# Kernel optimization log

Hardware: AMD Instinct MI355X
Metric: run time of the kernel (lower is better)

Reference implementation:

```python
import jax, jax.numpy as jnp
import numpy as np

EPS = 1.1920929e-07  # torch clamp_probs eps for float32
TEMP = 0.3           # sampler temperature T


def conv1d(x, w, b, pad):
    # x: [B, Cin, L], w: [Cout, Cin, K] -> [B, Cout, L']
    y = jax.lax.conv_general_dilated(x, w, window_strides=(1,), padding=[(pad, pad)],
                                     dimension_numbers=('NCH', 'OIH', 'NCH'))
    return y + b[None, :, None]


def setup_inputs() -> dict:
    key = jax.random.key(0)
    ks = jax.random.split(key, 20)
    B, L, V, E, F, H, K = 512, 512, 100000, 100, 100, 100, 10
    p = lambda i, shape: jax.random.normal(ks[i], shape, jnp.float32) * 0.02
    return {
        'x': jax.random.randint(ks[0], (B, L), 0, V, dtype=jnp.int32),
        'u': jax.random.uniform(ks[1], (B, K, L), dtype=jnp.float32),
        'emb': p(2, (V, E)),
        'conv1_w': p(3, (F, E, 3)), 'conv1_b': p(4, (F,)),
        'gi_w': p(5, (H, F)), 'gi_b': p(6, (H,)),
        'conv2_w': p(7, (H, F, 3)), 'conv2_b': p(8, (H,)),
        'li_w': p(9, (H, H, 3)), 'li_b': p(10, (H,)),
        'conv3_w': p(11, (F, 2 * H, 1)), 'conv3_b': p(12, (F,)),
        'conv4_w': p(13, (1, F, 1)), 'conv4_b': p(14, (1,)),
        'fc1_w': p(15, (H, E)), 'fc1_b': p(16, (H,)),
        'head_w': p(17, (1, H)), 'head_b': p(18, (1,)),
    }


def _ti_logits(e, conv1_w, conv1_b, gi_w, gi_b, conv2_w, conv2_b,
               li_w, li_b, conv3_w, conv3_b, conv4_w, conv4_b):
    relu = jax.nn.relu
    xt = jnp.swapaxes(e, 1, 2)                       # [B, E, L]
    h = relu(conv1d(xt, conv1_w, conv1_b, 1))        # [B, F, L]
    g = relu(h.mean(axis=-1) @ gi_w.T + gi_b)        # [B, H] (AdaptiveAvgPool1d(1))
    loc = relu(conv1d(relu(conv1d(h, conv2_w, conv2_b, 1)), li_w, li_b, 1))  # [B, H, L]
    gexp = jnp.broadcast_to(g[:, :, None], loc.shape)
    z = jnp.concatenate([gexp, loc], axis=1)         # [B, 2H, L]
    z = relu(conv1d(z, conv3_w, conv3_b, 0))
    return conv1d(z, conv4_w, conv4_b, 0)            # [B, 1, L]


def reference(x, u, emb, conv1_w, conv1_b, gi_w, gi_b, conv2_w, conv2_b,
              li_w, li_b, conv3_w, conv3_b, conv4_w, conv4_b,
              fc1_w, fc1_b, head_w, head_b):
    e = emb[x]                                       # [B, L, E] embedding gather
    logits = _ti_logits(e, conv1_w, conv1_b, gi_w, gi_b, conv2_w, conv2_b,
                        li_w, li_b, conv3_w, conv3_b, conv4_w, conv4_b)
    # Gumbel top-k continuous sampling (training path)
    uc = jnp.clip(u, EPS, 1.0 - EPS)
    gumbel = -jnp.log(-jnp.log(uc))                  # [B, K, L]
    noisy = (gumbel + logits) / TEMP                 # logits [B,1,L] broadcasts over K
    csamples = jax.nn.softmax(noisy, axis=-1).max(axis=1)  # [B, L]
    # distil predictor: masked mean pooling + MLP + sigmoid head
    pooled = (e * csamples[:, :, None]).mean(axis=1)  # [B, E]
    h = jax.nn.relu(pooled @ fc1_w.T + fc1_b)
    out = jax.nn.sigmoid(h @ head_w.T + head_b)       # [B, 1]
    return out, csamples
```

## Files before the change

kernel.cpp:

```cpp
#include <hip/hip_runtime.h>
#include <math.h>

#define DEV __device__ __forceinline__

typedef __attribute__((ext_vector_type(8))) short short8;
typedef __attribute__((ext_vector_type(4))) short short4v;
typedef __attribute__((ext_vector_type(4))) float f32x4;

#define SSTR 136

DEV short f2bf(float f) {
    unsigned u = __builtin_bit_cast(unsigned, f);
    unsigned r = (u + 0x7fffu + ((u >> 16) & 1u)) >> 16;
    return (short)r;
}

__global__ __launch_bounds__(256) void emb_cvt_kernel(
    const float* __restrict__ emb, short* __restrict__ embT) {
    int t = threadIdx.x;
    int row = blockIdx.x * 8 + (t >> 5);
    int c4 = t & 31;
    if (c4 >= 28) return;
    short4v v = {0, 0, 0, 0};
    if (c4 < 25) {
        f32x4 e = *(const f32x4*)&emb[row * 100 + c4 * 4];
#pragma unroll
        for (int r = 0; r < 4; ++r) v[r] = f2bf(e[r]);
    }
    *(short4v*)&embT[row * 112 + c4 * 4] = v;
}

__global__ __launch_bounds__(64) void pack_all_kernel(
    const float* __restrict__ c1w, const float* __restrict__ c2w,
    const float* __restrict__ liw, const float* __restrict__ c3w,
    short* __restrict__ A1, short* __restrict__ A2,
    short* __restrict__ A3, short* __restrict__ A4) {
    int bx = blockIdx.x;
    const float* w; short* dst; int mode, lbx;
    if (bx < 70)       { w = c1w; dst = A1; mode = 0; lbx = bx; }
    else if (bx < 140) { w = c2w; dst = A2; mode = 0; lbx = bx - 70; }
    else if (bx < 210) { w = liw; dst = A3; mode = 0; lbx = bx - 140; }
    else               { w = c3w; dst = A4; mode = 1; lbx = bx - 210; }
    int lane = threadIdx.x;
    int f = lbx % 7 * 16 + (lane & 15);
    int kb = (lbx / 7) * 32 + (lane >> 4) * 8;
    short8 v;
#pragma unroll
    for (int j = 0; j < 8; ++j) {
        int kk = kb + j;
        float val = 0.f;
        if (f < 100) {
            if (mode == 0) {
                int oct = kk >> 3, dk = oct / 13;
                int c = (oct - 13 * dk) * 8 + (kk & 7);
                if (dk < 3 && c < 100) val = w[(f * 100 + c) * 3 + dk];
            } else {
                if (kk < 100) val = w[f * 200 + 100 + kk];
            }
        }
        v[j] = f2bf(val);
    }
    *(short8*)&dst[(lbx * 64 + lane) * 8] = v;
}

template<int NT, bool POOL, bool TO_GLOBAL>
DEV void conv3tap(const short* __restrict__ Ap, const float* __restrict__ bias,
                  const short* s_src, short* s_dst, short* __restrict__ gout,
                  int row0l, int l0, float* __restrict__ hpart, int pbase,
                  int lane, int wv) {
    const int q = lane >> 4, n = lane & 15;
    const int mt0 = wv * 2;
    const bool two = (wv < 3);
    const f32x4 z4 = {0.f, 0.f, 0.f, 0.f};
    f32x4 acc0[NT], acc1[NT];
#pragma unroll
    for (int nt = 0; nt < NT; ++nt) { acc0[nt] = z4; acc1[nt] = z4; }
#pragma unroll
    for (int ks = 0; ks < 10; ++ks) {
        short8 a0 = *(const short8*)&Ap[(ks * 448 + mt0 * 64 + lane) * 8];
        short8 a1;
        if (two) a1 = *(const short8*)&Ap[(ks * 448 + (mt0 + 1) * 64 + lane) * 8];
        int oct = ks * 4 + q;
        int dk = oct / 13;
        int c0 = (oct - 13 * dk) * 8;
        const short* bptr = s_src + (n + dk) * SSTR + c0;
#pragma unroll
        for (int nt = 0; nt < NT; ++nt) {
            short8 bf;
            if (nt < 4) {
                bf = *(const short8*)(bptr + nt * 16 * SSTR);
            } else {
                int r = 64 + n + dk; if (r > 69) r = 69;
                bf = *(const short8*)&s_src[r * SSTR + c0];
            }
            acc0[nt] = __builtin_amdgcn_mfma_f32_16x16x32_bf16(a0, bf, acc0[nt], 0, 0, 0);
            if (two)
                acc1[nt] = __builtin_amdgcn_mfma_f32_16x16x32_bf16(a1, bf, acc1[nt], 0, 0, 0);
        }
    }
    const int fb0 = mt0 * 16 + q * 4;
    const int fb1 = fb0 + 16;
    f32x4 bs0 = (fb0 < 100) ? *(const f32x4*)&bias[fb0] : z4;
    f32x4 bs1 = (two && fb1 < 100) ? *(const f32x4*)&bias[fb1] : z4;
    f32x4 ps0 = z4, ps1 = z4;
#pragma unroll
    for (int nt = 0; nt < NT; ++nt) {
        const int j = nt * 16 + n;
        const int l = row0l + j;
        const bool lok = (l >= 0) && (l < 512);
        const bool pok = (l >= l0) && (l < l0 + 64);
        short4v pk0, pk1;
#pragma unroll
        for (int r = 0; r < 4; ++r) {
            float v0 = fmaxf(acc0[nt][r] + bs0[r], 0.f);
            v0 = lok ? v0 : 0.f;
            pk0[r] = f2bf(v0);
            if constexpr (POOL) { if (pok) ps0[r] += v0; }
            if (two) {
                float v1 = fmaxf(acc1[nt][r] + bs1[r], 0.f);
                v1 = lok ? v1 : 0.f;
                pk1[r] = f2bf(v1);
                if constexpr (POOL) { if (pok) ps1[r] += v1; }
            }
        }
        if constexpr (TO_GLOBAL) {
            if (j < 64) {
                *(short4v*)&gout[j * 112 + fb0] = pk0;
                if (two) *(short4v*)&gout[j * 112 + fb1] = pk1;
            }
        } else {
            if (j < 70) {
                *(short4v*)&s_dst[j * SSTR + fb0] = pk0;
                if (two) *(short4v*)&s_dst[j * SSTR + fb1] = pk1;
            }
        }
    }
    if constexpr (POOL) {
#pragma unroll
        for (int off = 1; off <= 8; off <<= 1)
#pragma unroll
            for (int r = 0; r < 4; ++r) {
                ps0[r] += __shfl_xor(ps0[r], off, 64);
                ps1[r] += __shfl_xor(ps1[r], off, 64);
            }
        if (n == 0) {
            *(f32x4*)&hpart[pbase * 112 + fb0] = ps0;
            if (two) *(f32x4*)&hpart[pbase * 112 + fb1] = ps1;
        }
    }
}

__global__ __launch_bounds__(256, 4) void fused_conv_kernel(
    const int* __restrict__ xidx, const short* __restrict__ embT,
    const short* __restrict__ A1, const short* __restrict__ A2,
    const short* __restrict__ A3,
    const float* __restrict__ b1, const float* __restrict__ b2,
    const float* __restrict__ b3,
    short* __restrict__ locT, float* __restrict__ hpart) {
    extern __shared__ char smem[];
    short* s_e = (short*)smem;
    short* s_h = (short*)(smem + 72 * SSTR * 2);
    const int tid = threadIdx.x;
    const int b = blockIdx.y, bx = blockIdx.x, l0 = bx * 64;
    const int lane = tid & 63, wv = tid >> 6;

#pragma unroll
    for (int p = 0; p < 5; ++p) {
        int idx = tid + p * 256;
        int j = idx >> 4, c8 = idx & 15;
        if (j < 70 && c8 < 14) {
            int lg = l0 - 3 + j;
            short8 v = {0, 0, 0, 0, 0, 0, 0, 0};
            if (lg >= 0 && lg < 512) {
                int row = xidx[b * 512 + lg];
                v = *(const short8*)&embT[row * 112 + c8 * 8];
            }
            *(short8*)&s_e[j * SSTR + c8 * 8] = v;
        }
    }
    __syncthreads();
    conv3tap<5, true, false>(A1, b1, s_e, s_h, nullptr, l0 - 2, l0,
                             hpart, b * 8 + bx, lane, wv);
    __syncthreads();
    conv3tap<5, false, false>(A2, b2, s_h, s_e, nullptr, l0 - 1, l0,
                              nullptr, 0, lane, wv);
    __syncthreads();
    conv3tap<4, false, true>(A3, b3, s_e, nullptr,
                             locT + ((size_t)b * 512 + l0) * 112, l0, l0,
                             nullptr, 0, lane, wv);
}

__global__ __launch_bounds__(256, 4) void conv3_logits_kernel(
    const short* __restrict__ locT, const short* __restrict__ A4,
    const float* __restrict__ zg, const float* __restrict__ w4,
    const float* __restrict__ b4, float* __restrict__ logits) {
    extern __shared__ char smem[];
    short* s_in = (short*)smem;
    float* s_part = (float*)(smem + 128 * SSTR * 2);
    const int tid = threadIdx.x;
    const int b = blockIdx.y, l0r = blockIdx.x * 128;
    const int lane = tid & 63, wv = tid >> 6;
    const int q = lane >> 4, n = lane & 15;

    {
        short8 tmp[8];
#pragma unroll
        for (int p = 0; p < 8; ++p) {
            int idx = tid + p * 256;
            int j = idx >> 4, c8 = idx & 15;
            if (c8 < 14)
                tmp[p] = *(const short8*)&locT[((size_t)b * 512 + l0r + j) * 112 + c8 * 8];
        }
#pragma unroll
        for (int p = 0; p < 8; ++p) {
            int idx = tid + p * 256;
            int j = idx >> 4, c8 = idx & 15;
            if (c8 < 14)
                *(short8*)&s_in[j * SSTR + c8 * 8] = tmp[p];
        }
    }
    __syncthreads();

    const f32x4 z4 = {0.f, 0.f, 0.f, 0.f};
    const int mt0 = wv * 2;
    const bool two = (wv < 3);
    f32x4 acc0[8], acc1[8];
#pragma unroll
    for (int nt = 0; nt < 8; ++nt) { acc0[nt] = z4; acc1[nt] = z4; }
#pragma unroll
    for (int ks = 0; ks < 4; ++ks) {
        short8 a0 = *(const short8*)&A4[(ks * 448 + mt0 * 64 + lane) * 8];
        short8 a1;
        if (two) a1 = *(const short8*)&A4[(ks * 448 + (mt0 + 1) * 64 + lane) * 8];
        int c0 = (ks * 4 + q) * 8;
        if (c0 > 104) c0 = 104;
        const short* bptr = s_in + n * SSTR + c0;
#pragma unroll
        for (int nt = 0; nt < 8; ++nt) {
            short8 bf = *(const short8*)(bptr + nt * 16 * SSTR);
            acc0[nt] = __builtin_amdgcn_mfma_f32_16x16x32_bf16(a0, bf, acc0[nt], 0, 0, 0);
            if (two)
                acc1[nt] = __builtin_amdgcn_mfma_f32_16x16x32_bf16(a1, bf, acc1[nt], 0, 0, 0);
        }
    }
    const int fb0 = mt0 * 16 + q * 4, fb1 = fb0 + 16;
    f32x4 w40 = (fb0 < 100) ? *(const f32x4*)&w4[fb0] : z4;
    f32x4 w41 = (two && fb1 < 100) ? *(const f32x4*)&w4[fb1] : z4;
    f32x4 zg0 = *(const f32x4*)&zg[b * 112 + fb0];
    f32x4 zg1 = two ? *(const f32x4*)&zg[b * 112 + fb1] : z4;
#pragma unroll
    for (int nt = 0; nt < 8; ++nt) {
        float part = 0.f;
#pragma unroll
        for (int r = 0; r < 4; ++r) {
            part += fmaxf(acc0[nt][r] + zg0[r], 0.f) * w40[r];
            if (two) part += fmaxf(acc1[nt][r] + zg1[r], 0.f) * w41[r];
        }
        part += __shfl_xor(part, 16, 64);
        part += __shfl_xor(part, 32, 64);
        if (q == 0) s_part[wv * 128 + nt * 16 + n] = part;
    }
    __syncthreads();
    if (tid < 128) {
        float s = s_part[tid] + s_part[128 + tid] + s_part[256 + tid] +
                  s_part[384 + tid] + b4[0];
        logits[b * 512 + l0r + tid] = s;
    }
}

__global__ __launch_bounds__(128) void pool_gate_kernel(
    const float* __restrict__ hpart, const float* __restrict__ gi_w,
    const float* __restrict__ gi_b, const float* __restrict__ w3,
    const float* __restrict__ b3, float* __restrict__ zg) {
    int b = blockIdx.x, tid = threadIdx.x;
    __shared__ float s_hm[112];
    __shared__ float s_g[100];
    if (tid < 112) {
        float a = 0.f;
#pragma unroll
        for (int s = 0; s < 8; ++s) a += hpart[(b * 8 + s) * 112 + tid];
        s_hm[tid] = a * (1.f / 512.f);
    }
    __syncthreads();
    if (tid < 100) {
        float a = gi_b[tid];
        for (int f = 0; f < 100; ++f) a += s_hm[f] * gi_w[tid * 100 + f];
        s_g[tid] = fmaxf(a, 0.f);
    }
    __syncthreads();
    if (tid < 112) {
        float a = 0.f;
        if (tid < 100) {
            a = b3[tid];
            for (int h = 0; h < 100; ++h) a += s_g[h] * w3[tid * 200 + h];
        }
        zg[b * 112 + tid] = a;
    }
}

__global__ __launch_bounds__(256) void sampler_kernel(
    const float* __restrict__ u, const float* __restrict__ logits,
    float* __restrict__ cs) {
    const float EPSV = 1.1920929e-07f;
    int b = blockIdx.x, tid = threadIdx.x;
    int lane = tid & 63, wv = tid >> 6;
    __shared__ float s_log[512], s_cs[512], s_red[8];
    float uu[20];
#pragma unroll
    for (int k = 0; k < 10; ++k) {
        uu[k * 2]     = u[(b * 10 + k) * 512 + tid];
        uu[k * 2 + 1] = u[(b * 10 + k) * 512 + tid + 256];
    }
    for (int l = tid; l < 512; l += 256) { s_log[l] = logits[b * 512 + l]; s_cs[l] = 0.f; }
    __syncthreads();
    for (int k = 0; k < 10; ++k) {
        float nz[2];
#pragma unroll
        for (int i = 0; i < 2; ++i) {
            int l = tid + i * 256;
            float vv = fminf(fmaxf(uu[k * 2 + i], EPSV), 1.f - EPSV);
            float g = -__logf(-__logf(vv));
            nz[i] = (g + s_log[l]) * (1.f / 0.3f);
        }
        float m = fmaxf(nz[0], nz[1]);
#pragma unroll
        for (int off = 32; off >= 1; off >>= 1) m = fmaxf(m, __shfl_xor(m, off, 64));
        if (lane == 0) s_red[wv] = m;
        __syncthreads();
        m = fmaxf(fmaxf(s_red[0], s_red[1]), fmaxf(s_red[2], s_red[3]));
        float e0 = __expf(nz[0] - m), e1 = __expf(nz[1] - m);
        float s = e0 + e1;
#pragma unroll
        for (int off = 32; off >= 1; off >>= 1) s += __shfl_xor(s, off, 64);
        if (lane == 0) s_red[4 + wv] = s;
        __syncthreads();
        float inv = 1.f / (s_red[4] + s_red[5] + s_red[6] + s_red[7]);
        s_cs[tid]       = fmaxf(s_cs[tid],       e0 * inv);
        s_cs[tid + 256] = fmaxf(s_cs[tid + 256], e1 * inv);
    }
    for (int l = tid; l < 512; l += 256) cs[b * 512 + l] = s_cs[l];
}

__global__ __launch_bounds__(256) void head_part_kernel(
    const int* __restrict__ xidx, const float* __restrict__ emb,
    const float* __restrict__ cs, float* __restrict__ hp) {
    int sb = blockIdx.x, b = blockIdx.y;
    int tid = threadIdx.x;
    __shared__ int s_x[64];
    __shared__ float s_c[64];
    __shared__ float s_acc[8][104];
    if (tid < 64) {
        int l = sb * 64 + tid;
        s_x[tid] = xidx[b * 512 + l];
        s_c[tid] = cs[b * 512 + l];
    }
    __syncthreads();
    int s = tid & 31, lq = tid >> 5;
    if (s < 25) {
        f32x4 a = {0.f, 0.f, 0.f, 0.f};
#pragma unroll
        for (int i = 0; i < 8; ++i) {
            int ll = lq * 8 + i;
            int row = s_x[ll];
            float cv = s_c[ll];
            f32x4 ev = *(const f32x4*)&emb[row * 100 + s * 4];
#pragma unroll
            for (int r = 0; r < 4; ++r) a[r] += ev[r] * cv;
        }
        *(f32x4*)&s_acc[lq][s * 4] = a;
    }
    __syncthreads();
    if (tid < 100) {
        float v = 0.f;
#pragma unroll
        for (int j = 0; j < 8; ++j) v += s_acc[j][tid];
        hp[(b * 8 + sb) * 100 + tid] = v;
    }
}

__global__ __launch_bounds__(128) void head_fin_kernel(
    const float* __restrict__ hp, const float* __restrict__ fc1_w,
    const float* __restrict__ fc1_b, const float* __restrict__ head_w,
    const float* __restrict__ head_b, float* __restrict__ out) {
    int b = blockIdx.x, tid = threadIdx.x;
    int lane = tid & 63, wv = tid >> 6;
    __shared__ float s_pool[100];
    __shared__ float s_h2[100];
    __shared__ float s_red[2];
    if (tid < 100) {
        float a = 0.f;
#pragma unroll
        for (int sb = 0; sb < 8; ++sb) a += hp[(b * 8 + sb) * 100 + tid];
        s_pool[tid] = a * (1.f / 512.f);
    }
    __syncthreads();
    if (tid < 100) {
        float acc = fc1_b[tid];
        for (int i = 0; i < 100; ++i) acc += s_pool[i] * fc1_w[tid * 100 + i];
        s_h2[tid] = fmaxf(acc, 0.f);
    }
    __syncthreads();
    float v = (tid < 100) ? s_h2[tid] * head_w[tid] : 0.f;
#pragma unroll
    for (int off = 32; off >= 1; off >>= 1) v += __shfl_xor(v, off, 64);
    if (lane == 0) s_red[wv] = v;
    __syncthreads();
    if (tid == 0) {
        float z = s_red[0] + s_red[1] + head_b[0];
        out[b] = 1.f / (1.f + __expf(-z));
    }
}

extern "C" void kernel_launch(void* const* d_in, const int* in_sizes, int n_in,
                              void* d_out, int out_size, void* d_ws, size_t ws_size,
                              hipStream_t stream) {
    const int*   x   = (const int*)d_in[0];
    const float* u   = (const float*)d_in[1];
    const float* emb = (const float*)d_in[2];
    const float* c1w = (const float*)d_in[3];
    const float* c1b = (const float*)d_in[4];
    const float* giw = (const float*)d_in[5];
    const float* gib = (const float*)d_in[6];
    const float* c2w = (const float*)d_in[7];
    const float* c2b = (const float*)d_in[8];
    const float* liw = (const float*)d_in[9];
    const float* lib = (const float*)d_in[10];
    const float* c3w = (const float*)d_in[11];
    const float* c3b = (const float*)d_in[12];
    const float* c4w = (const float*)d_in[13];
    const float* c4b = (const float*)d_in[14];
    const float* f1w = (const float*)d_in[15];
    const float* f1b = (const float*)d_in[16];
    const float* hww = (const float*)d_in[17];
    const float* hbb = (const float*)d_in[18];
    float* out = (float*)d_out;

    char* ws = (char*)d_ws;
    short* locT   = (short*)(ws + 0);
    short* embT   = (short*)(ws + 58720256);
    short* A1     = (short*)(ws + 81120256);
    short* A2     = (short*)(ws + 81191936);
    short* A3     = (short*)(ws + 81263616);
    short* A4     = (short*)(ws + 81335296);
    float* zg     = (float*)(ws + 81363968);
    float* logits = (float*)(ws + 81593344);
    float* hpart  = (float*)(ws + 82641920);
    float* hp     = (float*)(ws + 84476928);

    emb_cvt_kernel<<<12500, 256, 0, stream>>>(emb, embT);
    pack_all_kernel<<<238, 64, 0, stream>>>(c1w, c2w, liw, c3w, A1, A2, A3, A4);

    size_t smemA = 2 * 72 * SSTR * 2;
    fused_conv_kernel<<<dim3(8, 512), 256, smemA, stream>>>(
        x, embT, A1, A2, A3, c1b, c2b, lib, locT, hpart);
    pool_gate_kernel<<<512, 128, 0, stream>>>(hpart, giw, gib, c3w, c3b, zg);
    size_t smemB = 128 * SSTR * 2 + 4 * 128 * 4;
    conv3_logits_kernel<<<dim3(4, 512), 256, smemB, stream>>>(
        locT, A4, zg, c4w, c4b, logits);
    sampler_kernel<<<512, 256, 0, stream>>>(u, logits, out + 512);
    head_part_kernel<<<dim3(8, 512), 256, 0, stream>>>(x, emb, out + 512, hp);
    head_fin_kernel<<<512, 128, 0, stream>>>(hp, f1w, f1b, hww, hbb, out);
}
```

Measured before the change: 288.1 us.

## Fuse sampler and head kernels, fold biases into MFMA accumulators, specialize edge tiles

Merges the sampler, head_part and head_fin kernels into one per-batch kernel. The pooled embedding sum now reads the bf16 embT table instead of fp32 emb, which removes two launches and the hp round trip through global memory. In the conv kernels, biases and the gate term are used as the initial accumulator values, and B-operand LDS offsets are precomputed once. A template variant skips the boundary masking for interior tiles, and a packed bf16 convert instruction is used when the builtin exists. The trade-off is that pooling now uses bf16-rounded embeddings, which changes numerics slightly, and the fused head runs with only 512 blocks.

```diff
diff --git a/kernel.cpp b/kernel.cpp
--- a/kernel.cpp
+++ b/kernel.cpp
@@ -6,6 +6,7 @@
 typedef __attribute__((ext_vector_type(8))) short short8;
 typedef __attribute__((ext_vector_type(4))) short short4v;
 typedef __attribute__((ext_vector_type(4))) float f32x4;
+typedef __attribute__((ext_vector_type(2))) unsigned uint2v;
 
 #define SSTR 136
 
@@ -13,6 +14,23 @@
     unsigned u = __builtin_bit_cast(unsigned, f);
     unsigned r = (u + 0x7fffu + ((u >> 16) & 1u)) >> 16;
     return (short)r;
+}
+
+#if __has_builtin(__builtin_amdgcn_cvt_pk_bf16_f32)
+DEV unsigned pk2bf(float a, float b) {
+    auto v = __builtin_amdgcn_cvt_pk_bf16_f32(a, b);
+    return __builtin_bit_cast(unsigned, v);
+}
+#else
+DEV unsigned pk2bf(float a, float b) {
+    return ((unsigned)(unsigned short)f2bf(a)) |
+           (((unsigned)(unsigned short)f2bf(b)) << 16);
+}
+#endif
+
+DEV float bfu(short s) {
+    unsigned u = ((unsigned)(unsigned short)s) << 16;
+    return __builtin_bit_cast(float, u);
 }
 
 __global__ __launch_bounds__(256) void emb_cvt_kernel(
@@ -63,9 +81,11 @@
     *(short8*)&dst[(lbx * 64 + lane) * 8] = v;
 }
 
-template<int NT, bool POOL, bool TO_GLOBAL>
-DEV void conv3tap(const short* __restrict__ Ap, const float* __restrict__ bias,
-                  const short* s_src, short* s_dst, short* __restrict__ gout,
+template<int NT, bool POOL, bool TO_GLOBAL, bool EDGE>
+DEV void conv3tap(const short* __restrict__ Ap, const short* s_src,
+                  short* s_dst, short* __restrict__ gout,
+                  const int* bofs, const int* bofs4,
+                  const f32x4 bs0, const f32x4 bs1,
                   int row0l, int l0, float* __restrict__ hpart, int pbase,
                   int lane, int wv) {
     const int q = lane >> 4, n = lane & 15;
@@ -74,64 +94,63 @@
     const f32x4 z4 = {0.f, 0.f, 0.f, 0.f};
     f32x4 acc0[NT], acc1[NT];
 #pragma unroll
-    for (int nt = 0; nt < NT; ++nt) { acc0[nt] = z4; acc1[nt] = z4; }
+    for (int nt = 0; nt < NT; ++nt) { acc0[nt] = bs0; acc1[nt] = bs1; }
 #pragma unroll
     for (int ks = 0; ks < 10; ++ks) {
         short8 a0 = *(const short8*)&Ap[(ks * 448 + mt0 * 64 + lane) * 8];
         short8 a1;
         if (two) a1 = *(const short8*)&Ap[(ks * 448 + (mt0 + 1) * 64 + lane) * 8];
-        int oct = ks * 4 + q;
-        int dk = oct / 13;
-        int c0 = (oct - 13 * dk) * 8;
-        const short* bptr = s_src + (n + dk) * SSTR + c0;
+        const char* bp = (const char*)s_src + bofs[ks];
 #pragma unroll
         for (int nt = 0; nt < NT; ++nt) {
             short8 bf;
-            if (nt < 4) {
-                bf = *(const short8*)(bptr + nt * 16 * SSTR);
-            } else {
-                int r = 64 + n + dk; if (r > 69) r = 69;
-                bf = *(const short8*)&s_src[r * SSTR + c0];
-            }
+            if (nt < 4) bf = *(const short8*)(bp + nt * (16 * SSTR * 2));
+            else        bf = *(const short8*)((const char*)s_src + bofs4[ks]);
             acc0[nt] = __builtin_amdgcn_mfma_f32_16x16x32_bf16(a0, bf, acc0[nt], 0, 0, 0);
             if (two)
                 acc1[nt] = __builtin_amdgcn_mfma_f32_16x16x32_bf16(a1, bf, acc1[nt], 0, 0, 0);
         }
     }
-    const int fb0 = mt0 * 16 + q * 4;
-    const int fb1 = fb0 + 16;
-    f32x4 bs0 = (fb0 < 100) ? *(const f32x4*)&bias[fb0] : z4;
-    f32x4 bs1 = (two && fb1 < 100) ? *(const f32x4*)&bias[fb1] : z4;
+    const int fb0 = mt0 * 16 + q * 4, fb1 = fb0 + 16;
     f32x4 ps0 = z4, ps1 = z4;
 #pragma unroll
     for (int nt = 0; nt < NT; ++nt) {
         const int j = nt * 16 + n;
-        const int l = row0l + j;
-        const bool lok = (l >= 0) && (l < 512);
-        const bool pok = (l >= l0) && (l < l0 + 64);
-        short4v pk0, pk1;
+        f32x4 v0, v1;
 #pragma unroll
         for (int r = 0; r < 4; ++r) {
-            float v0 = fmaxf(acc0[nt][r] + bs0[r], 0.f);
-            v0 = lok ? v0 : 0.f;
-            pk0[r] = f2bf(v0);
-            if constexpr (POOL) { if (pok) ps0[r] += v0; }
-            if (two) {
-                float v1 = fmaxf(acc1[nt][r] + bs1[r], 0.f);
-                v1 = lok ? v1 : 0.f;
-                pk1[r] = f2bf(v1);
-                if constexpr (POOL) { if (pok) ps1[r] += v1; }
-            }
-        }
+            v0[r] = fmaxf(acc0[nt][r], 0.f);
+            if (two) v1[r] = fmaxf(acc1[nt][r], 0.f);
+        }
+        if constexpr (EDGE) {
+            const bool lok = (unsigned)(row0l + j) < 512u;
+#pragma unroll
+            for (int r = 0; r < 4; ++r) {
+                v0[r] = lok ? v0[r] : 0.f;
+                if (two) v1[r] = lok ? v1[r] : 0.f;
+            }
+        }
+        if constexpr (POOL) {
+            const int l = row0l + j;
+            const bool pok = (l >= l0) && (l < l0 + 64);
+            if (pok) {
+#pragma unroll
+                for (int r = 0; r < 4; ++r) {
+                    ps0[r] += v0[r];
+                    if (two) ps1[r] += v1[r];
+                }
+            }
+        }
+        uint2v pk0, pk1;
+        pk0[0] = pk2bf(v0[0], v0[1]); pk0[1] = pk2bf(v0[2], v0[3]);
+        if (two) { pk1[0] = pk2bf(v1[0], v1[1]); pk1[1] = pk2bf(v1[2], v1[3]); }
         if constexpr (TO_GLOBAL) {
-            if (j < 64) {
-                *(short4v*)&gout[j * 112 + fb0] = pk0;
-                if (two) *(short4v*)&gout[j * 112 + fb1] = pk1;
-            }
+            *(uint2v*)&gout[j * 112 + fb0] = pk0;
+            if (two) *(uint2v*)&gout[j * 112 + fb1] = pk1;
         } else {
-            if (j < 70) {
-                *(short4v*)&s_dst[j * SSTR + fb0] = pk0;
-                if (two) *(short4v*)&s_dst[j * SSTR + fb1] = pk1;
+            if (nt < 4 || n < 6) {
+                *(uint2v*)&s_dst[j * SSTR + fb0] = pk0;
+                if (two) *(uint2v*)&s_dst[j * SSTR + fb1] = pk1;
             }
         }
     }
@@ -163,6 +182,7 @@
     const int tid = threadIdx.x;
     const int b = blockIdx.y, bx = blockIdx.x, l0 = bx * 64;
     const int lane = tid & 63, wv = tid >> 6;
+    const int q = lane >> 4, n = lane & 15;
 
 #pragma unroll
     for (int p = 0; p < 5; ++p) {
@@ -178,16 +198,50 @@
             *(short8*)&s_e[j * SSTR + c8 * 8] = v;
         }
     }
-    __syncthreads();
-    conv3tap<5, true, false>(A1, b1, s_e, s_h, nullptr, l0 - 2, l0,
-                             hpart, b * 8 + bx, lane, wv);
-    __syncthreads();
-    conv3tap<5, false, false>(A2, b2, s_h, s_e, nullptr, l0 - 1, l0,
-                              nullptr, 0, lane, wv);
-    __syncthreads();
-    conv3tap<4, false, true>(A3, b3, s_e, nullptr,
-                             locT + ((size_t)b * 512 + l0) * 112, l0, l0,
-                             nullptr, 0, lane, wv);
+
+    int bofs[10], bofs4[10];
+#pragma unroll
+    for (int ks = 0; ks < 10; ++ks) {
+        int oct = ks * 4 + q;
+        int dk = (oct >= 39) ? 3 : (oct >= 26) ? 2 : (oct >= 13) ? 1 : 0;
+        int c0 = (oct - 13 * dk) * 8;
+        bofs[ks] = ((n + dk) * SSTR + c0) * 2;
+        int r4 = 64 + n + dk; if (r4 > 69) r4 = 69;
+        bofs4[ks] = (r4 * SSTR + c0) * 2;
+    }
+    const int fb0 = wv * 32 + q * 4, fb1 = fb0 + 16;
+    const f32x4 z4 = {0.f, 0.f, 0.f, 0.f};
+    f32x4 bsA0 = (fb0 < 100) ? *(const f32x4*)&b1[fb0] : z4;
+    f32x4 bsA1 = (fb1 < 100) ? *(const f32x4*)&b1[fb1] : z4;
+    f32x4 bsB0 = (fb0 < 100) ? *(const f32x4*)&b2[fb0] : z4;
+    f32x4 bsB1 = (fb1 < 100) ? *(const f32x4*)&b2[fb1] : z4;
+    f32x4 bsC0 = (fb0 < 100) ? *(const f32x4*)&b3[fb0] : z4;
+    f32x4 bsC1 = (fb1 < 100) ? *(const f32x4*)&b3[fb1] : z4;
+
+    __syncthreads();
+    const bool edge = (bx == 0) || (bx == 7);
+    if (edge) {
+        conv3tap<5, true, false, true>(A1, s_e, s_h, nullptr, bofs, bofs4,
+                                       bsA0, bsA1, l0 - 2, l0, hpart,
+                                       b * 8 + bx, lane, wv);
+        __syncthreads();
+        conv3tap<5, false, false, true>(A2, s_h, s_e, nullptr, bofs, bofs4,
+                                        bsB0, bsB1, l0 - 1, l0, nullptr, 0,
+                                        lane, wv);
+    } else {
+        conv3tap<5, true, false, false>(A1, s_e, s_h, nullptr, bofs, bofs4,
+                                        bsA0, bsA1, l0 - 2, l0, hpart,
+                                        b * 8 + bx, lane, wv);
+        __syncthreads();
+        conv3tap<5, false, false, false>(A2, s_h, s_e, nullptr, bofs, bofs4,
+                                         bsB0, bsB1, l0 - 1, l0, nullptr, 0,
+                                         lane, wv);
+    }
+    __syncthreads();
+    conv3tap<4, false, true, false>(A3, s_e, nullptr,
+                                    locT + ((size_t)b * 512 + l0) * 112,
+                                    bofs, bofs4, bsC0, bsC1, l0, l0,
+                                    nullptr, 0, lane, wv);
 }
 
 __global__ __launch_bounds__(256, 4) void conv3_logits_kernel(
@@ -219,14 +273,17 @@
                 *(short8*)&s_in[j * SSTR + c8 * 8] = tmp[p];
         }
     }
-    __syncthreads();
-
     const f32x4 z4 = {0.f, 0.f, 0.f, 0.f};
     const int mt0 = wv * 2;
     const bool two = (wv < 3);
+    const int fb0 = mt0 * 16 + q * 4, fb1 = fb0 + 16;
+    f32x4 zg0 = *(const f32x4*)&zg[b * 112 + fb0];
+    f32x4 zg1 = two ? *(const f32x4*)&zg[b * 112 + fb1] : z4;
     f32x4 acc0[8], acc1[8];
 #pragma unroll
-    for (int nt = 0; nt < 8; ++nt) { acc0[nt] = z4; acc1[nt] = z4; }
+    for (int nt = 0; nt < 8; ++nt) { acc0[nt] = zg0; acc1[nt] = zg1; }
+    __syncthreads();
+
 #pragma unroll
     for (int ks = 0; ks < 4; ++ks) {
         short8 a0 = *(const short8*)&A4[(ks * 448 + mt0 * 64 + lane) * 8];
@@ -243,18 +300,15 @@
                 acc1[nt] = __builtin_amdgcn_mfma_f32_16x16x32_bf16(a1, bf, acc1[nt], 0, 0, 0);
         }
     }
-    const int fb0 = mt0 * 16 + q * 4, fb1 = fb0 + 16;
     f32x4 w40 = (fb0 < 100) ? *(const f32x4*)&w4[fb0] : z4;
     f32x4 w41 = (two && fb1 < 100) ? *(const f32x4*)&w4[fb1] : z4;
-    f32x4 zg0 = *(const f32x4*)&zg[b * 112 + fb0];
-    f32x4 zg1 = two ? *(const f32x4*)&zg[b * 112 + fb1] : z4;
 #pragma unroll
     for (int nt = 0; nt < 8; ++nt) {
         float part = 0.f;
 #pragma unroll
         for (int r = 0; r < 4; ++r) {
-            part += fmaxf(acc0[nt][r] + zg0[r], 0.f) * w40[r];
-            if (two) part += fmaxf(acc1[nt][r] + zg1[r], 0.f) * w41[r];
+            part += fmaxf(acc0[nt][r], 0.f) * w40[r];
+            if (two) part += fmaxf(acc1[nt][r], 0.f) * w41[r];
         }
         part += __shfl_xor(part, 16, 64);
         part += __shfl_xor(part, 32, 64);
@@ -298,20 +352,30 @@
     }
 }
 
-__global__ __launch_bounds__(256) void sampler_kernel(
+__global__ __launch_bounds__(256) void samp_head_kernel(
     const float* __restrict__ u, const float* __restrict__ logits,
-    float* __restrict__ cs) {
+    const int* __restrict__ xidx, const short* __restrict__ embT,
+    const float* __restrict__ f1w, const float* __restrict__ f1b,
+    const float* __restrict__ hw, const float* __restrict__ hb,
+    float* __restrict__ cs_out, float* __restrict__ out) {
     const float EPSV = 1.1920929e-07f;
     int b = blockIdx.x, tid = threadIdx.x;
     int lane = tid & 63, wv = tid >> 6;
     __shared__ float s_log[512], s_cs[512], s_red[8];
+    __shared__ int s_x[512];
+    __shared__ float s_acc[16][112];
+    __shared__ float s_pool[112], s_h2[100], s_fin[4];
     float uu[20];
 #pragma unroll
     for (int k = 0; k < 10; ++k) {
         uu[k * 2]     = u[(b * 10 + k) * 512 + tid];
         uu[k * 2 + 1] = u[(b * 10 + k) * 512 + tid + 256];
     }
-    for (int l = tid; l < 512; l += 256) { s_log[l] = logits[b * 512 + l]; s_cs[l] = 0.f; }
+    for (int l = tid; l < 512; l += 256) {
+        s_log[l] = logits[b * 512 + l];
+        s_cs[l] = 0.f;
+        s_x[l] = xidx[b * 512 + l];
+    }
     __syncthreads();
     for (int k = 0; k < 10; ++k) {
         float nz[2];
@@ -338,75 +402,46 @@
         s_cs[tid]       = fmaxf(s_cs[tid],       e0 * inv);
         s_cs[tid + 256] = fmaxf(s_cs[tid + 256], e1 * inv);
     }
-    for (int l = tid; l < 512; l += 256) cs[b * 512 + l] = s_cs[l];
-}
-
-__global__ __launch_bounds__(256) void head_part_kernel(
-    const int* __restrict__ xidx, const float* __restrict__ emb,
-    const float* __restrict__ cs, float* __restrict__ hp) {
-    int sb = blockIdx.x, b = blockIdx.y;
-    int tid = threadIdx.x;
-    __shared__ int s_x[64];
-    __shared__ float s_c[64];
-    __shared__ float s_acc[8][104];
-    if (tid < 64) {
-        int l = sb * 64 + tid;
-        s_x[tid] = xidx[b * 512 + l];
-        s_c[tid] = cs[b * 512 + l];
-    }
-    __syncthreads();
-    int s = tid & 31, lq = tid >> 5;
-    if (s < 25) {
-        f32x4 a = {0.f, 0.f, 0.f, 0.f};
-#pragma unroll
-        for (int i = 0; i < 8; ++i) {
-            int ll = lq * 8 + i;
-            int row = s_x[ll];
-            float cv = s_c[ll];
-            f32x4 ev = *(const f32x4*)&emb[row * 100 + s * 4];
-#pragma unroll
-            for (int r = 0; r < 4; ++r) a[r] += ev[r] * cv;
-        }
-        *(f32x4*)&s_acc[lq][s * 4] = a;
+    for (int l = tid; l < 512; l += 256) cs_out[b * 512 + l] = s_cs[l];
+    __syncthreads();
+    int jg = tid >> 4, c8 = tid & 15;
+    if (c8 < 14) {
+        f32x4 pa = {0.f, 0.f, 0.f, 0.f}, pb = {0.f, 0.f, 0.f, 0.f};
+#pragma unroll 4
+        for (int l = jg; l < 512; l += 16) {
+            int row = s_x[l];
+            float cv = s_cs[l];
+            short8 e8 = *(const short8*)&embT[(size_t)row * 112 + c8 * 8];
+#pragma unroll
+            for (int r = 0; r < 4; ++r) {
+                pa[r] += cv * bfu(e8[r]);
+                pb[r] += cv * bfu(e8[4 + r]);
+            }
+        }
+        *(f32x4*)&s_acc[jg][c8 * 8] = pa;
+        *(f32x4*)&s_acc[jg][c8 * 8 + 4] = pb;
+    }
+    __syncthreads();
+    if (tid < 112) {
+        float p = 0.f;
+#pragma unroll
+        for (int g = 0; g < 16; ++g) p += s_acc[g][tid];
+        s_pool[tid] = p * (1.f / 512.f);
     }
     __syncthreads();
     if (tid < 100) {
-        float v = 0.f;
-#pragma unroll
-        for (int j = 0; j < 8; ++j) v += s_acc[j][tid];
-        hp[(b * 8 + sb) * 100 + tid] = v;
-    }
-}
-
-__global__ __launch_bounds__(128) void head_fin_kernel(
-    const float* __restrict__ hp, const float* __restrict__ fc1_w,
-    const float* __restrict__ fc1_b, const float* __restrict__ head_w,
-    const float* __restrict__ head_b, float* __restrict__ out) {
-    int b = blockIdx.x, tid = threadIdx.x;
-    int lane = tid & 63, wv = tid >> 6;
-    __shared__ float s_pool[100];
-    __shared__ float s_h2[100];
-    __shared__ float s_red[2];
-    if (tid < 100) {
-        float a = 0.f;
-#pragma unroll
-        for (int sb = 0; sb < 8; ++sb) a += hp[(b * 8 + sb) * 100 + tid];
-        s_pool[tid] = a * (1.f / 512.f);
-    }
-    __syncthreads();
-    if (tid < 100) {
-        float acc = fc1_b[tid];
-        for (int i = 0; i < 100; ++i) acc += s_pool[i] * fc1_w[tid * 100 + i];
-        s_h2[tid] = fmaxf(acc, 0.f);
-    }
-    __syncthreads();
-    float v = (tid < 100) ? s_h2[tid] * head_w[tid] : 0.f;
+        float a = f1b[tid];
+        for (int i = 0; i < 100; ++i) a += s_pool[i] * f1w[tid * 100 + i];
+        s_h2[tid] = fmaxf(a, 0.f);
+    }
+    __syncthreads();
+    float v = (tid < 100) ? s_h2[tid] * hw[tid] : 0.f;
 #pragma unroll
     for (int off = 32; off >= 1; off >>= 1) v += __shfl_xor(v, off, 64);
-    if (lane == 0) s_red[wv] = v;
+    if (lane == 0) s_fin[wv] = v;
     __syncthreads();
     if (tid == 0) {
-        float z = s_red[0] + s_red[1] + head_b[0];
+        float z = s_fin[0] + s_fin[1] + s_fin[2] + s_fin[3] + hb[0];
         out[b] = 1.f / (1.f + __expf(-z));
     }
 }
@@ -445,7 +480,6 @@
     float* zg     = (float*)(ws + 81363968);
     float* logits = (float*)(ws + 81593344);
     float* hpart  = (float*)(ws + 82641920);
-    float* hp     = (float*)(ws + 84476928);
 
     emb_cvt_kernel<<<12500, 256, 0, stream>>>(emb, embT);
     pack_all_kernel<<<238, 64, 0, stream>>>(c1w, c2w, liw, c3w, A1, A2, A3, A4);
@@ -457,7 +491,6 @@
     size_t smemB = 128 * SSTR * 2 + 4 * 128 * 4;
     conv3_logits_kernel<<<dim3(4, 512), 256, smemB, stream>>>(
         locT, A4, zg, c4w, c4b, logits);
-    sampler_kernel<<<512, 256, 0, stream>>>(u, logits, out + 512);
-    head_part_kernel<<<dim3(8, 512), 256, 0, stream>>>(x, emb, out + 512, hp);
-    head_fin_kernel<<<512, 128, 0, stream>>>(hp, f1w, f1b, hww, hbb, out);
-}
+    samp_head_kernel<<<512, 256, 0, stream>>>(
+        u, logits, x, embT, f1w, f1b, hww, hbb, out + 512, out);
+}
```

After: 277.2 us. 3.8% less time.
